# Performance work log

Hardware: AMD Instinct MI355X
Metric: run time of the kernel (lower is better)

Reference implementation:

```python
import jax, jax.numpy as jnp
import numpy as np

_D = (-2, -1)  # (height, width) axes for rot90


def _tl(top, lft, p):
    # top-left corner where no HPX face exists; blend top's left cols and lft's top rows
    ret = jnp.zeros(top.shape[:-2] + (p, p), top.dtype)
    ret = ret.at[..., -1, -1].set(0.5 * top[..., -1, 0] + 0.5 * lft[..., 0, -1])
    for i in range(1, p):
        ret = ret.at[..., -i - 1, -i:].set(top[..., -i - 1, :i])
        ret = ret.at[..., -i:, -i - 1].set(lft[..., :i, -i - 1])
        ret = ret.at[..., -i - 1, -i - 1].set(0.5 * top[..., -i - 1, 0] + 0.5 * lft[..., 0, -i - 1])
    return ret


def _br(b, r, p):
    # bottom-right corner where no HPX face exists (mirror of _tl)
    ret = jnp.zeros(b.shape[:-2] + (p, p), b.dtype)
    ret = ret.at[..., 0, 0].set(0.5 * b[..., 0, -1] + 0.5 * r[..., -1, 0])
    for i in range(1, p):
        ret = ret.at[..., i, :i].set(b[..., i, -i:])
        ret = ret.at[..., :i, i].set(r[..., -i:, i])
        ret = ret.at[..., i, i].set(0.5 * b[..., i, -1] + 0.5 * r[..., -1, i])
    return ret


def _pn(c, t, tl, lft, bl, b, br, rgt, tr, p):
    cc = jnp.concatenate((jnp.rot90(t, 1, _D)[..., -p:, :], c, b[..., :p, :]), axis=-2)
    left = jnp.concatenate((jnp.rot90(tl, 2, _D)[..., -p:, -p:], jnp.rot90(lft, -1, _D)[..., -p:], bl[..., :p, -p:]), axis=-2)
    right = jnp.concatenate((tr[..., -p:, :p], rgt[..., :p], br[..., :p, :p]), axis=-2)
    return jnp.concatenate((left, cc, right), axis=-1)


def _pe(c, t, tl, lft, bl, b, br, rgt, tr, p):
    cc = jnp.concatenate((t[..., -p:, :], c, b[..., :p, :]), axis=-2)
    left = jnp.concatenate((tl[..., -p:, -p:], lft[..., -p:], bl[..., :p, -p:]), axis=-2)
    right = jnp.concatenate((tr[..., -p:, :p], rgt[..., :p], br[..., :p, :p]), axis=-2)
    return jnp.concatenate((left, cc, right), axis=-1)


def _ps(c, t, tl, lft, bl, b, br, rgt, tr, p):
    cc = jnp.concatenate((t[..., -p:, :], c, jnp.rot90(b, 1, _D)[..., :p, :]), axis=-2)
    left = jnp.concatenate((tl[..., -p:, -p:], lft[..., -p:], bl[..., :p, -p:]), axis=-2)
    right = jnp.concatenate((tr[..., -p:, :p], jnp.rot90(rgt, -1, _D)[..., :p], jnp.rot90(br, 2, _D)[..., :p, :p]), axis=-2)
    return jnp.concatenate((left, cc, right), axis=-1)


def _healpix_pad(data, p):
    NF, C, H, W = data.shape
    x = data.reshape(NF // 12, 12, C, H, W)
    f = [x[:, i] for i in range(12)]
    (f00, f01, f02, f03, f04, f05, f06, f07, f08, f09, f10, f11) = f
    p00 = _pn(f00, f01, f02, f03, f03, f04, f08, f05, f01, p)
    p01 = _pn(f01, f02, f03, f00, f00, f05, f09, f06, f02, p)
    p02 = _pn(f02, f03, f00, f01, f01, f06, f10, f07, f03, p)
    p03 = _pn(f03, f00, f01, f02, f02, f07, f11, f04, f00, p)
    p04 = _pe(f04, f00, _tl(f00, f03, p), f03, f07, f11, _br(f11, f08, p), f08, f05, p)
    p05 = _pe(f05, f01, _tl(f01, f00, p), f00, f04, f08, _br(f08, f09, p), f09, f06, p)
    p06 = _pe(f06, f02, _tl(f02, f01, p), f01, f05, f09, _br(f09, f10, p), f10, f07, p)
    p07 = _pe(f07, f03, _tl(f03, f02, p), f02, f06, f10, _br(f10, f11, p), f11, f04, p)
    p08 = _ps(f08, f05, f00, f04, f11, f11, f10, f09, f09, p)
    p09 = _ps(f09, f06, f01, f05, f08, f08, f11, f10, f10, p)
    p10 = _ps(f10, f07, f02, f06, f09, f09, f08, f11, f11, p)
    p11 = _ps(f11, f04, f03, f07, f10, f10, f09, f08, f08, p)
    res = jnp.stack((p00, p01, p02, p03, p04, p05, p06, p07, p08, p09, p10, p11), axis=1)
    return res.reshape(NF, C, H + 2 * p, W + 2 * p)


def setup_inputs() -> dict:
    key = jax.random.key(0)
    data = jax.random.normal(key, (96, 256, 64, 64), dtype=jnp.float32)  # [B*12, C, H, W]
    return {"data": data, "p": 2}


def reference(data, p):
    return _healpix_pad(data, p)
```

## Files before the change

kernel.cpp:

```cpp
#include <hip/hip_runtime.h>
#include <cstdint>

#define NB 8
#define NC 256
#define FH 64
#define OW 68
#define IMG_IN 4096
#define IMG_OUT 4624
#define N_IMG 24576
#define HALO 528

__device__ const int c_tT[12]  = {1,2,3,0,  0,1,2,3,  5,6,7,4};
__device__ const int c_tTL[12] = {2,3,0,1,  0,0,0,0,  0,1,2,3};
__device__ const int c_tL[12]  = {3,0,1,2,  3,0,1,2,  4,5,6,7};
__device__ const int c_tBL[12] = {3,0,1,2,  7,4,5,6,  11,8,9,10};
__device__ const int c_tB[12]  = {4,5,6,7,  11,8,9,10, 11,8,9,10};
__device__ const int c_tBR[12] = {8,9,10,11, 0,0,0,0,  10,11,8,9};
__device__ const int c_tR[12]  = {5,6,7,4,  8,9,10,11, 9,10,11,8};
__device__ const int c_tTR[12] = {1,2,3,0,  5,6,7,4,  9,10,11,8};

__global__ __launch_bounds__(256) void interior_copy(const float* __restrict__ in,
                                                     float* __restrict__ out) {
    int t = blockIdx.x * 256 + threadIdx.x;
    int n  = t >> 11;
    int r  = t & 2047;
    int y  = r >> 5;
    int c2 = r & 31;
    const float2* s = reinterpret_cast<const float2*>(in + n * IMG_IN + y * 64) + c2;
    float2 v = *s;
    float2* d = reinterpret_cast<float2*>(out + n * IMG_OUT + (y + 2) * OW + 2) + c2;
    *d = v;
}

__device__ __forceinline__ float halo_value(const float* __restrict__ in,
                                            int bb, int ch, int fi,
                                            int oy, int ox) {
    auto ld = [&](int face, int sy, int sx) -> float {
        return in[(((bb * 12 + face) * NC + ch) * IMG_IN) + sy * 64 + sx];
    };

    const int y = oy - 2;
    const int x = ox - 2;
    const int rx = (ox < 2) ? 0 : (ox < 66 ? 1 : 2);
    const int ry = (oy < 2) ? 0 : (oy < 66 ? 1 : 2);
    const int ft = fi >> 2;

    float v = 0.0f;

    if (ft == 0) {
        if (ry == 0) {
            if (rx == 1)      v = ld(c_tT[fi], x, 1 - oy);
            else if (rx == 0) v = ld(c_tTL[fi], 1 - oy, 1 - ox);
            else              v = ld(c_tTR[fi], 62 + oy, x - 64);
        } else if (ry == 1) {
            if (rx == 0)      v = ld(c_tL[fi], 1 - ox, y);
            else              v = ld(c_tR[fi], y, x - 64);
        } else {
            if (rx == 1)      v = ld(c_tB[fi], y - 64, x);
            else if (rx == 0) v = ld(c_tBL[fi], y - 64, 62 + ox);
            else              v = ld(c_tBR[fi], y - 64, x - 64);
        }
    } else if (ft == 1) {
        if (ry == 0) {
            if (rx == 1)      v = ld(c_tT[fi], 62 + oy, x);
            else if (rx == 2) v = ld(c_tTR[fi], 62 + oy, x - 64);
            else {
                int r = oy, c = ox;
                if (c > r)      v = ld(c_tT[fi], 62 + r, c - r - 1);
                else if (r > c) v = ld(c_tL[fi], r - c - 1, 62 + c);
                else            v = 0.5f * (ld(c_tT[fi], 62 + r, 0) +
                                            ld(c_tL[fi], 0, 62 + r));
            }
        } else if (ry == 1) {
            if (rx == 0)      v = ld(c_tL[fi], y, 62 + ox);
            else              v = ld(c_tR[fi], y, x - 64);
        } else {
            if (rx == 1)      v = ld(c_tB[fi], y - 64, x);
            else if (rx == 0) v = ld(c_tBL[fi], y - 64, 62 + ox);
            else {
                int r = y - 64, c = x - 64;
                if (r > c)      v = ld(c_tB[fi], r, 64 - r + c);
                else if (c > r) v = ld(c_tR[fi], 64 - c + r, c);
                else            v = 0.5f * (ld(c_tB[fi], r, 63) +
                                            ld(c_tR[fi], 63, r));
            }
        }
    } else {
        if (ry == 0) {
            if (rx == 1)      v = ld(c_tT[fi], 62 + oy, x);
            else if (rx == 0) v = ld(c_tTL[fi], 62 + oy, 62 + ox);
            else              v = ld(c_tTR[fi], 62 + oy, x - 64);
        } else if (ry == 1) {
            if (rx == 0)      v = ld(c_tL[fi], y, 62 + ox);
            else              v = ld(c_tR[fi], 127 - x, y);
        } else {
            if (rx == 1)      v = ld(c_tB[fi], x, 127 - y);
            else if (rx == 0) v = ld(c_tBL[fi], y - 64, 62 + ox);
            else              v = ld(c_tBR[fi], 127 - y, 127 - x);
        }
    }
    return v;
}

__global__ __launch_bounds__(256) void halo_fill(const float* __restrict__ in,
                                                 float* __restrict__ out) {
    int idx = blockIdx.x * 256 + threadIdx.x;
    if (idx >= N_IMG * HALO) return;

    int n   = idx / HALO;
    int hid = idx - n * HALO;
    int nf  = n >> 8;
    int ch  = n & 255;
    int bb  = nf / 12;
    int fi  = nf - bb * 12;

    int oy, ox;
    if (hid < 272) {
        oy = hid / 68;
        ox = hid - oy * 68;
        oy += (oy >> 1) << 6;
    } else {
        int h = hid - 272;
        oy = 2 + (h >> 2);
        int c = h & 3;
        ox = c + ((c >> 1) << 6);
    }

    float v = halo_value(in, bb, ch, fi, oy, ox);
    out[n * IMG_OUT + oy * OW + ox] = v;
}

extern "C" void kernel_launch(void* const* d_in, const int* in_sizes, int n_in,
                              void* d_out, int out_size, void* d_ws, size_t ws_size,
                              hipStream_t stream) {
    const float* in = (const float*)d_in[0];
    float* out = (float*)d_out;

    const int n_int_blocks = (N_IMG * 2048) / 256;
    interior_copy<<<n_int_blocks, 256, 0, stream>>>(in, out);

    const int n_halo_blocks = (N_IMG * HALO) / 256;
    halo_fill<<<n_halo_blocks, 256, 0, stream>>>(in, out);
}
```

Before: 900.7 us.

## Fuse interior copy and halo fill into one per-image kernel with vector stores

```diff
diff --git a/kernel.cpp b/kernel.cpp
--- a/kernel.cpp
+++ b/kernel.cpp
@@ -8,7 +8,9 @@
 #define IMG_IN 4096
 #define IMG_OUT 4624
 #define N_IMG 24576
-#define HALO 528
+#define Q_PER_IMG 1156
+
+typedef float f32x4 __attribute__((ext_vector_type(4)));
 
 __device__ const int c_tT[12]  = {1,2,3,0,  0,1,2,3,  5,6,7,4};
 __device__ const int c_tTL[12] = {2,3,0,1,  0,0,0,0,  0,1,2,3};
@@ -18,19 +20,6 @@
 __device__ const int c_tBR[12] = {8,9,10,11, 0,0,0,0,  10,11,8,9};
 __device__ const int c_tR[12]  = {5,6,7,4,  8,9,10,11, 9,10,11,8};
 __device__ const int c_tTR[12] = {1,2,3,0,  5,6,7,4,  9,10,11,8};
-
-__global__ __launch_bounds__(256) void interior_copy(const float* __restrict__ in,
-                                                     float* __restrict__ out) {
-    int t = blockIdx.x * 256 + threadIdx.x;
-    int n  = t >> 11;
-    int r  = t & 2047;
-    int y  = r >> 5;
-    int c2 = r & 31;
-    const float2* s = reinterpret_cast<const float2*>(in + n * IMG_IN + y * 64) + c2;
-    float2 v = *s;
-    float2* d = reinterpret_cast<float2*>(out + n * IMG_OUT + (y + 2) * OW + 2) + c2;
-    *d = v;
-}
 
 __device__ __forceinline__ float halo_value(const float* __restrict__ in,
                                             int bb, int ch, int fi,
@@ -102,32 +91,47 @@
     return v;
 }
 
-__global__ __launch_bounds__(256) void halo_fill(const float* __restrict__ in,
+__global__ __launch_bounds__(256) void fused_pad(const float* __restrict__ in,
                                                  float* __restrict__ out) {
-    int idx = blockIdx.x * 256 + threadIdx.x;
-    if (idx >= N_IMG * HALO) return;
+    const int img = blockIdx.x;
+    const int nf  = img >> 8;
+    const int ch  = img & 255;
+    const int bb  = nf / 12;
+    const int fi  = nf - bb * 12;
+    const float* __restrict__ base = in + (size_t)img * IMG_IN;
+    f32x4* __restrict__ obase =
+        reinterpret_cast<f32x4*>(out + (size_t)img * IMG_OUT);
+    const int tid = threadIdx.x;
 
-    int n   = idx / HALO;
-    int hid = idx - n * HALO;
-    int nf  = n >> 8;
-    int ch  = n & 255;
-    int bb  = nf / 12;
-    int fi  = nf - bb * 12;
+    auto process = [&](int q) {
+        const int oy  = q / 17;
+        const int ox0 = (q - oy * 17) << 2;
+        f32x4 v;
+        if (oy >= 2 && oy < 66 && ox0 >= 4 && ox0 < 64) {
+            const float* s = base + (oy - 2) * 64 + (ox0 - 2);
+            const float2 a = *reinterpret_cast<const float2*>(s);
+            const float2 b = *reinterpret_cast<const float2*>(s + 2);
+            v.x = a.x; v.y = a.y; v.z = b.x; v.w = b.y;
+        } else {
+#pragma unroll
+            for (int k = 0; k < 4; ++k) {
+                const int ox = ox0 + k;
+                float e;
+                if (oy >= 2 && oy < 66 && ox >= 2 && ox < 66)
+                    e = base[(oy - 2) * 64 + (ox - 2)];
+                else
+                    e = halo_value(in, bb, ch, fi, oy, ox);
+                v[k] = e;
+            }
+        }
+        __builtin_nontemporal_store(v, obase + q);
+    };
 
-    int oy, ox;
-    if (hid < 272) {
-        oy = hid / 68;
-        ox = hid - oy * 68;
-        oy += (oy >> 1) << 6;
-    } else {
-        int h = hid - 272;
-        oy = 2 + (h >> 2);
-        int c = h & 3;
-        ox = c + ((c >> 1) << 6);
-    }
-
-    float v = halo_value(in, bb, ch, fi, oy, ox);
-    out[n * IMG_OUT + oy * OW + ox] = v;
+#pragma unroll
+    for (int i = 0; i < 4; ++i)
+        process(tid + i * 256);
+    if (tid < Q_PER_IMG - 1024)
+        process(tid + 1024);
 }
 
 extern "C" void kernel_launch(void* const* d_in, const int* in_sizes, int n_in,
@@ -135,10 +139,5 @@
                               hipStream_t stream) {
     const float* in = (const float*)d_in[0];
     float* out = (float*)d_out;
-
-    const int n_int_blocks = (N_IMG * 2048) / 256;
-    interior_copy<<<n_int_blocks, 256, 0, stream>>>(in, out);
-
-    const int n_halo_blocks = (N_IMG * HALO) / 256;
-    halo_fill<<<n_halo_blocks, 256, 0, stream>>>(in, out);
+    fused_pad<<<N_IMG, 256, 0, stream>>>(in, out);
 }
```

Measured after the change: 833.8 us. 7.4% less time.
